# Optimization experiments

Hardware: AMD Instinct MI355X
Metric: run time of the kernel (lower is better)

## Reference

```python
import jax, jax.numpy as jnp
import numpy as np

N = 50000
E = 800000
C_IN = 256
HEADS = 4
HEAD_DIM = 32  # out_channels per head; concat=False -> final dim = HEAD_DIM


def setup_inputs() -> dict:
    key = jax.random.key(0)
    ks = jax.random.split(key, 10)
    s_in = 1.0 / np.sqrt(C_IN)
    return {
        "x": jax.random.normal(ks[0], (N, C_IN), dtype=jnp.float32),
        "edge_index": jax.random.randint(ks[1], (2, E), 0, N, dtype=jnp.int64),
        "Wq": jax.random.normal(ks[2], (C_IN, HEADS * HEAD_DIM), dtype=jnp.float32) * s_in,
        "bq": jax.random.normal(ks[3], (HEADS * HEAD_DIM,), dtype=jnp.float32) * 0.02,
        "Wk": jax.random.normal(ks[4], (C_IN, HEADS * HEAD_DIM), dtype=jnp.float32) * s_in,
        "bk": jax.random.normal(ks[5], (HEADS * HEAD_DIM,), dtype=jnp.float32) * 0.02,
        "Wv": jax.random.normal(ks[6], (C_IN, HEADS * HEAD_DIM), dtype=jnp.float32) * s_in,
        "bv": jax.random.normal(ks[7], (HEADS * HEAD_DIM,), dtype=jnp.float32) * 0.02,
        "Ws": jax.random.normal(ks[8], (C_IN, HEAD_DIM), dtype=jnp.float32) * s_in,
        "bs": jax.random.normal(ks[9], (HEAD_DIM,), dtype=jnp.float32) * 0.02,
    }


def reference(x, edge_index, Wq, bq, Wk, bk, Wv, bv, Ws, bs):
    n = x.shape[0]
    # Node-level projections, reshaped to (N, H, C)
    q = (x @ Wq + bq).reshape(n, HEADS, HEAD_DIM)
    k = (x @ Wk + bk).reshape(n, HEADS, HEAD_DIM)
    v = (x @ Wv + bv).reshape(n, HEADS, HEAD_DIM)

    src, dst = edge_index[0], edge_index[1]
    # Per-edge attention logits: (E, H)
    scale = 1.0 / jnp.sqrt(jnp.asarray(HEAD_DIM, dtype=x.dtype))
    logits = jnp.einsum("ehc,ehc->eh", q[dst], k[src]) * scale

    # Segment softmax over incoming edges of each destination node
    m = jax.ops.segment_max(logits, dst, num_segments=n)  # (N, H)
    e = jnp.exp(logits - m[dst])
    s = jax.ops.segment_sum(e, dst, num_segments=n)  # (N, H)
    alpha = e / s[dst]  # (E, H)

    # Weighted scatter-sum of values: (N, H, C)
    out = jax.ops.segment_sum(v[src] * alpha[..., None], dst, num_segments=n)
    # concat=False -> mean over heads; root skip connection
    out = out.mean(axis=1) + x @ Ws + bs  # (N, C)
    # LeakyReLU(0.1)
    return jnp.where(out > 0, out, 0.1 * out)
```

## Files before the change

### kernel.cpp

```cpp
#include <hip/hip_runtime.h>
#include <hip/hip_bf16.h>

#define NN 50000
#define EE 800000
#define CIN 256
#define HEADS 4
#define HDIM 32
#define GBM 64
#define CAP 64

typedef float f32x4 __attribute__((ext_vector_type(4)));
typedef __bf16 bf16x8 __attribute__((ext_vector_type(8)));

typedef const __attribute__((address_space(1))) unsigned int* gptr_t;
typedef __attribute__((address_space(3))) unsigned int* lptr_t;

static __device__ __forceinline__ unsigned short f2b(float f) {
    __hip_bfloat16 h = __float2bfloat16(f);
    return *(unsigned short*)&h;
}
static __device__ __forceinline__ float blo(unsigned int u) {
    union { unsigned int i; float f; } c; c.i = u << 16; return c.f;
}
static __device__ __forceinline__ float bhi(unsigned int u) {
    union { unsigned int i; float f; } c; c.i = u & 0xffff0000u; return c.f;
}

__global__ __launch_bounds__(256) void prep_w(
    const float* __restrict__ Wq, const float* __restrict__ Wk,
    const float* __restrict__ Wv, const float* __restrict__ Ws,
    unsigned short* __restrict__ WT) {
    const int t = blockIdx.x * 256 + threadIdx.x;
    if (t >= 416 * 256) return;
    const int c = t >> 8;
    const int k = t & 255;
    float w;
    if (c < 128)      w = Wq[k * 128 + c];
    else if (c < 256) w = Wk[k * 128 + (c - 128)];
    else if (c < 384) w = Wv[k * 128 + (c - 256)];
    else              w = Ws[k * 32 + (c - 384)];
    WT[t] = f2b(w);
}

__global__ __launch_bounds__(256) void mfma_gemm(
    const float* __restrict__ x, const unsigned short* __restrict__ WT,
    const float* __restrict__ bq, const float* __restrict__ bk,
    const float* __restrict__ bv, const float* __restrict__ bs,
    unsigned short* __restrict__ qb, unsigned short* __restrict__ kb,
    unsigned short* __restrict__ vb, float* __restrict__ skip) {
    __shared__ __align__(16) __hip_bfloat16 As[GBM * 256];
    __shared__ __align__(16) __hip_bfloat16 Bs[2][32 * 256];

    const int row0 = blockIdx.x * GBM;
    const int tid = threadIdx.x;
    const int wave = tid >> 6;
    const int lane = tid & 63;
    const int lr = lane & 15;
    const int lq = lane >> 4;

    #pragma unroll
    for (int i = 0; i < 8; ++i) {
        const int u = i * 256 + tid;
        const int r = u >> 5, cc = u & 31;
        int grow = row0 + r; if (grow >= NN) grow = NN - 1;
        const float4 f0 = *(const float4*)(x + (size_t)grow * CIN + cc * 8);
        const float4 f1 = *(const float4*)(x + (size_t)grow * CIN + cc * 8 + 4);
        union { unsigned short us[8]; uint4 v; } o;
        o.us[0] = f2b(f0.x); o.us[1] = f2b(f0.y); o.us[2] = f2b(f0.z); o.us[3] = f2b(f0.w);
        o.us[4] = f2b(f1.x); o.us[5] = f2b(f1.y); o.us[6] = f2b(f1.z); o.us[7] = f2b(f1.w);
        *(uint4*)(As + (r * 32 + (cc ^ (r & 7))) * 8) = o.v;
    }

    auto stageB = [&](int ct, int buf) {
        const int col0 = ct * 32;
        #pragma unroll
        for (int i = 0; i < 4; ++i) {
            const int u = i * 256 + tid;
            const int cB = u >> 5;
            const int ccs = (u & 31) ^ (cB & 7);
            __builtin_amdgcn_global_load_lds(
                (gptr_t)(const void*)(WT + (size_t)(col0 + cB) * CIN + ccs * 8),
                (lptr_t)(void*)(&Bs[buf][0] + (size_t)(i * 256 + (tid & 0xC0)) * 8),
                16, 0, 0);
        }
    };

    stageB(0, 0);
    __syncthreads();

    bf16x8 af[8];
    #pragma unroll
    for (int ks = 0; ks < 8; ++ks) {
        const int r = wave * 16 + lr;
        const int c = (ks * 4 + lq) ^ (lr & 7);
        af[ks] = *(const bf16x8*)(As + (r * 32 + c) * 8);
    }

    for (int ct = 0; ct < 13; ++ct) {
        const int cur = ct & 1;
        if (ct < 12) stageB(ct + 1, cur ^ 1);

        const int col0 = ct * 32;
        f32x4 acc[2] = {};
        #pragma unroll
        for (int ks = 0; ks < 8; ++ks) {
            const int cc = ks * 4 + lq;
            const bf16x8 b0 = *(const bf16x8*)(&Bs[cur][0] +
                (size_t)((lr * 32 + (cc ^ (lr & 7))) * 8));
            const bf16x8 b1 = *(const bf16x8*)(&Bs[cur][0] +
                (size_t)(((16 + lr) * 32 + (cc ^ (lr & 7))) * 8));
            acc[0] = __builtin_amdgcn_mfma_f32_16x16x32_bf16(af[ks], b0, acc[0], 0, 0, 0);
            acc[1] = __builtin_amdgcn_mfma_f32_16x16x32_bf16(af[ks], b1, acc[1], 0, 0, 0);
        }

        #pragma unroll
        for (int j = 0; j < 2; ++j)
            #pragma unroll
            for (int r = 0; r < 4; ++r) {
                const int grow = row0 + wave * 16 + lq * 4 + r;
                if (grow >= NN) continue;
                const int gcol = col0 + j * 16 + lr;
                const float val = acc[j][r];
                if (gcol < 128)
                    qb[(size_t)grow * 128 + gcol] = f2b(val + bq[gcol]);
                else if (gcol < 256)
                    kb[(size_t)grow * 128 + gcol - 128] = f2b(val + bk[gcol - 128]);
                else if (gcol < 384)
                    vb[(size_t)grow * 128 + gcol - 256] = f2b(val + bv[gcol - 256]);
                else
                    skip[(size_t)grow * 32 + gcol - 384] = val + bs[gcol - 384];
            }
        __syncthreads();
    }
}

__global__ __launch_bounds__(256) void fill_slots(const int* __restrict__ ei,
                                                  int* __restrict__ cnt,
                                                  unsigned short* __restrict__ slot) {
    const int t = blockIdx.x * 256 + threadIdx.x;
    if (t >= EE) return;
    const int dst = ei[EE + t];
    const int pos = atomicAdd(&cnt[dst], 1);
    if (pos < CAP) slot[(size_t)dst * CAP + pos] = (unsigned short)ei[t];
}

__global__ __launch_bounds__(256) void fused_edge(
    const unsigned short* __restrict__ qb, const unsigned short* __restrict__ kb,
    const unsigned short* __restrict__ vb, const unsigned short* __restrict__ slot,
    const int* __restrict__ cnt, const float* __restrict__ skip,
    float* __restrict__ out) {
    const int wid = blockIdx.x * 4 + (threadIdx.x >> 6);
    if (wid >= NN) return;
    const int lane = threadIdx.x & 63;
    const int sub = lane & 15;
    const int e4 = lane >> 4;

    const uint4 qu = *(const uint4*)(qb + (size_t)wid * 128 + sub * 8);
    float qf[8];
    qf[0] = blo(qu.x); qf[1] = bhi(qu.x); qf[2] = blo(qu.y); qf[3] = bhi(qu.y);
    qf[4] = blo(qu.z); qf[5] = bhi(qu.z); qf[6] = blo(qu.w); qf[7] = bhi(qu.w);

    const int deg = min(cnt[wid], CAP);
    const unsigned short* sl = slot + (size_t)wid * CAP;

    float s = 0.f;
    float acc[8] = {0.f, 0.f, 0.f, 0.f, 0.f, 0.f, 0.f, 0.f};

    for (int p0 = 0; p0 < deg; p0 += 4) {
        const int pe = p0 + e4;
        const bool valid = pe < deg;
        const int src = sl[valid ? pe : 0];
        const uint4 ku = *(const uint4*)(kb + (size_t)src * 128 + sub * 8);
        const uint4 vu = *(const uint4*)(vb + (size_t)src * 128 + sub * 8);

        float d = qf[0] * blo(ku.x) + qf[1] * bhi(ku.x)
                + qf[2] * blo(ku.y) + qf[3] * bhi(ku.y)
                + qf[4] * blo(ku.z) + qf[5] * bhi(ku.z)
                + qf[6] * blo(ku.w) + qf[7] * bhi(ku.w);
        d += __shfl_xor(d, 1);
        d += __shfl_xor(d, 2);
        const float w = valid ? __expf(d * 0.17677669529663687f) : 0.f;
        s += w;
        acc[0] += w * blo(vu.x); acc[1] += w * bhi(vu.x);
        acc[2] += w * blo(vu.y); acc[3] += w * bhi(vu.y);
        acc[4] += w * blo(vu.z); acc[5] += w * bhi(vu.z);
        acc[6] += w * blo(vu.w); acc[7] += w * bhi(vu.w);
    }

    s += __shfl_xor(s, 16); s += __shfl_xor(s, 32);
    #pragma unroll
    for (int j = 0; j < 8; ++j) {
        acc[j] += __shfl_xor(acc[j], 16);
        acc[j] += __shfl_xor(acc[j], 32);
    }
    const float inv = (s > 0.f) ? 0.25f / s : 0.f;
    #pragma unroll
    for (int j = 0; j < 8; ++j) acc[j] *= inv;
    #pragma unroll
    for (int j = 0; j < 8; ++j) {
        acc[j] += __shfl_xor(acc[j], 4);
        acc[j] += __shfl_xor(acc[j], 8);
    }

    if (lane < 4) {
        const float4 sk0 = *(const float4*)(skip + (size_t)wid * 32 + lane * 8);
        const float4 sk1 = *(const float4*)(skip + (size_t)wid * 32 + lane * 8 + 4);
        float o[8];
        o[0] = acc[0] + sk0.x; o[1] = acc[1] + sk0.y;
        o[2] = acc[2] + sk0.z; o[3] = acc[3] + sk0.w;
        o[4] = acc[4] + sk1.x; o[5] = acc[5] + sk1.y;
        o[6] = acc[6] + sk1.z; o[7] = acc[7] + sk1.w;
        #pragma unroll
        for (int j = 0; j < 8; ++j) o[j] = o[j] > 0.f ? o[j] : 0.1f * o[j];
        *(float4*)(out + (size_t)wid * 32 + lane * 8)     = make_float4(o[0], o[1], o[2], o[3]);
        *(float4*)(out + (size_t)wid * 32 + lane * 8 + 4) = make_float4(o[4], o[5], o[6], o[7]);
    }
}

extern "C" void kernel_launch(void* const* d_in, const int* in_sizes, int n_in,
                              void* d_out, int out_size, void* d_ws, size_t ws_size,
                              hipStream_t stream) {
    const float* x  = (const float*)d_in[0];
    const int*   ei = (const int*)d_in[1];
    const float* Wq = (const float*)d_in[2];
    const float* bq = (const float*)d_in[3];
    const float* Wk = (const float*)d_in[4];
    const float* bk = (const float*)d_in[5];
    const float* Wv = (const float*)d_in[6];
    const float* bv = (const float*)d_in[7];
    const float* Ws = (const float*)d_in[8];
    const float* bs = (const float*)d_in[9];
    float* out = (float*)d_out;

    char* ws = (char*)d_ws;
    size_t off = 0;
    auto alloc = [&](size_t bytes) { void* p = ws + off; off = (off + bytes + 255) & ~(size_t)255; return p; };
    unsigned short* WT   = (unsigned short*)alloc((size_t)416 * CIN * 2);
    unsigned short* qb   = (unsigned short*)alloc((size_t)NN * 128 * 2);
    unsigned short* kb   = (unsigned short*)alloc((size_t)NN * 128 * 2);
    unsigned short* vb   = (unsigned short*)alloc((size_t)NN * 128 * 2);
    float*          skip = (float*)alloc((size_t)NN * HDIM * 4);
    int*            cnt  = (int*)alloc((size_t)NN * 4);
    unsigned short* slot = (unsigned short*)alloc((size_t)NN * CAP * 2);

    hipMemsetAsync(cnt, 0, (size_t)NN * 4, stream);

    prep_w<<<(416 * 256 + 255) / 256, 256, 0, stream>>>(Wq, Wk, Wv, Ws, WT);

    fill_slots<<<(EE + 255) / 256, 256, 0, stream>>>(ei, cnt, slot);

    mfma_gemm<<<(NN + GBM - 1) / GBM, 256, 0, stream>>>(x, WT, bq, bk, bv, bs, qb, kb, vb, skip);

    fused_edge<<<(NN + 3) / 4, 256, 0, stream>>>(qb, kb, vb, slot, cnt, skip, out);
}
```

Baseline: 258.4 us.

## Stage GEMM outputs through LDS for coalesced vector stores, load A into registers

The projection GEMM now keeps all 13 column-tile accumulators in registers and writes them after the main loop, staging bf16 results (packed in pairs via lane shuffles) and fp32 skip values into a reused LDS buffer. From there each thread emits 16-byte row-contiguous stores, replacing the scattered 2-byte and 4-byte global stores that each needed bias loads and branches. The A tile is loaded straight from global into registers without an LDS round trip, and the biases are concatenated once in prep_w and cached in LDS. Holding 104 accumulator floats per thread raises register pressure, and launch_bounds(256,2) plus the 72 KB LDS footprint may limit occupancy or cause spills.

```diff
diff --git a/kernel.cpp b/kernel.cpp
--- a/kernel.cpp
+++ b/kernel.cpp
@@ -9,6 +9,10 @@
 #define GBM 64
 #define CAP 64
 
+#define OFF_C32 61440
+#define OFF_BIAS 70656
+#define LDS_BYTES 72320
+
 typedef float f32x4 __attribute__((ext_vector_type(4)));
 typedef __bf16 bf16x8 __attribute__((ext_vector_type(8)));
 
@@ -29,7 +33,9 @@
 __global__ __launch_bounds__(256) void prep_w(
     const float* __restrict__ Wq, const float* __restrict__ Wk,
     const float* __restrict__ Wv, const float* __restrict__ Ws,
-    unsigned short* __restrict__ WT) {
+    const float* __restrict__ bq, const float* __restrict__ bk,
+    const float* __restrict__ bv, const float* __restrict__ bs,
+    unsigned short* __restrict__ WT, float* __restrict__ bias_cat) {
     const int t = blockIdx.x * 256 + threadIdx.x;
     if (t >= 416 * 256) return;
     const int c = t >> 8;
@@ -40,16 +46,22 @@
     else if (c < 384) w = Wv[k * 128 + (c - 256)];
     else              w = Ws[k * 32 + (c - 384)];
     WT[t] = f2b(w);
-}
-
-__global__ __launch_bounds__(256) void mfma_gemm(
+    if (k == 0) {
+        float b;
+        if (c < 128)      b = bq[c];
+        else if (c < 256) b = bk[c - 128];
+        else if (c < 384) b = bv[c - 256];
+        else              b = bs[c - 384];
+        bias_cat[c] = b;
+    }
+}
+
+__global__ __launch_bounds__(256, 2) void mfma_gemm(
     const float* __restrict__ x, const unsigned short* __restrict__ WT,
-    const float* __restrict__ bq, const float* __restrict__ bk,
-    const float* __restrict__ bv, const float* __restrict__ bs,
+    const float* __restrict__ bias_cat,
     unsigned short* __restrict__ qb, unsigned short* __restrict__ kb,
     unsigned short* __restrict__ vb, float* __restrict__ skip) {
-    __shared__ __align__(16) __hip_bfloat16 As[GBM * 256];
-    __shared__ __align__(16) __hip_bfloat16 Bs[2][32 * 256];
+    __shared__ __align__(16) char U[LDS_BYTES];
 
     const int row0 = blockIdx.x * GBM;
     const int tid = threadIdx.x;
@@ -58,17 +70,21 @@
     const int lr = lane & 15;
     const int lq = lane >> 4;
 
-    #pragma unroll
-    for (int i = 0; i < 8; ++i) {
-        const int u = i * 256 + tid;
-        const int r = u >> 5, cc = u & 31;
-        int grow = row0 + r; if (grow >= NN) grow = NN - 1;
-        const float4 f0 = *(const float4*)(x + (size_t)grow * CIN + cc * 8);
-        const float4 f1 = *(const float4*)(x + (size_t)grow * CIN + cc * 8 + 4);
-        union { unsigned short us[8]; uint4 v; } o;
+    float* biasL = (float*)(U + OFF_BIAS);
+    for (int i = tid; i < 416; i += 256) biasL[i] = bias_cat[i];
+
+    int grow_a = row0 + wave * 16 + lr;
+    if (grow_a >= NN) grow_a = NN - 1;
+    const float* xr = x + (size_t)grow_a * CIN;
+    bf16x8 af[8];
+    #pragma unroll
+    for (int ks = 0; ks < 8; ++ks) {
+        const float4 f0 = *(const float4*)(xr + ks * 32 + lq * 8);
+        const float4 f1 = *(const float4*)(xr + ks * 32 + lq * 8 + 4);
+        union { unsigned short us[8]; bf16x8 v; } o;
         o.us[0] = f2b(f0.x); o.us[1] = f2b(f0.y); o.us[2] = f2b(f0.z); o.us[3] = f2b(f0.w);
         o.us[4] = f2b(f1.x); o.us[5] = f2b(f1.y); o.us[6] = f2b(f1.z); o.us[7] = f2b(f1.w);
-        *(uint4*)(As + (r * 32 + (cc ^ (r & 7))) * 8) = o.v;
+        af[ks] = o.v;
     }
 
     auto stageB = [&](int ct, int buf) {
@@ -80,7 +96,7 @@
             const int ccs = (u & 31) ^ (cB & 7);
             __builtin_amdgcn_global_load_lds(
                 (gptr_t)(const void*)(WT + (size_t)(col0 + cB) * CIN + ccs * 8),
-                (lptr_t)(void*)(&Bs[buf][0] + (size_t)(i * 256 + (tid & 0xC0)) * 8),
+                (lptr_t)(void*)(U + buf * 16384 + (i * 256 + (tid & 0xC0)) * 16),
                 16, 0, 0);
         }
     };
@@ -88,49 +104,72 @@
     stageB(0, 0);
     __syncthreads();
 
-    bf16x8 af[8];
-    #pragma unroll
-    for (int ks = 0; ks < 8; ++ks) {
-        const int r = wave * 16 + lr;
-        const int c = (ks * 4 + lq) ^ (lr & 7);
-        af[ks] = *(const bf16x8*)(As + (r * 32 + c) * 8);
-    }
-
+    f32x4 acc[13][2] = {};
+    #pragma unroll
     for (int ct = 0; ct < 13; ++ct) {
-        const int cur = ct & 1;
-        if (ct < 12) stageB(ct + 1, cur ^ 1);
-
-        const int col0 = ct * 32;
-        f32x4 acc[2] = {};
+        if (ct < 12) stageB(ct + 1, (ct & 1) ^ 1);
+        const unsigned short* Bc = (const unsigned short*)(U + (ct & 1) * 16384);
         #pragma unroll
         for (int ks = 0; ks < 8; ++ks) {
             const int cc = ks * 4 + lq;
-            const bf16x8 b0 = *(const bf16x8*)(&Bs[cur][0] +
-                (size_t)((lr * 32 + (cc ^ (lr & 7))) * 8));
-            const bf16x8 b1 = *(const bf16x8*)(&Bs[cur][0] +
-                (size_t)(((16 + lr) * 32 + (cc ^ (lr & 7))) * 8));
-            acc[0] = __builtin_amdgcn_mfma_f32_16x16x32_bf16(af[ks], b0, acc[0], 0, 0, 0);
-            acc[1] = __builtin_amdgcn_mfma_f32_16x16x32_bf16(af[ks], b1, acc[1], 0, 0, 0);
-        }
-
-        #pragma unroll
-        for (int j = 0; j < 2; ++j)
+            const bf16x8 b0 = *(const bf16x8*)(Bc + ((lr)      * 32 + (cc ^ (lr & 7))) * 8);
+            const bf16x8 b1 = *(const bf16x8*)(Bc + ((16 + lr) * 32 + (cc ^ (lr & 7))) * 8);
+            acc[ct][0] = __builtin_amdgcn_mfma_f32_16x16x32_bf16(af[ks], b0, acc[ct][0], 0, 0, 0);
+            acc[ct][1] = __builtin_amdgcn_mfma_f32_16x16x32_bf16(af[ks], b1, acc[ct][1], 0, 0, 0);
+        }
+        __syncthreads();
+    }
+
+    unsigned short* C16 = (unsigned short*)U;
+    float* C32 = (float*)(U + OFF_C32);
+    const int rbase = wave * 16 + lq * 4;
+    const int odd = lane & 1;
+    #pragma unroll
+    for (int ct = 0; ct < 12; ++ct) {
+        #pragma unroll
+        for (int j = 0; j < 2; ++j) {
+            const float bme = biasL[ct * 32 + j * 16 + lr];
+            unsigned int pr[4];
             #pragma unroll
             for (int r = 0; r < 4; ++r) {
-                const int grow = row0 + wave * 16 + lq * 4 + r;
-                if (grow >= NN) continue;
-                const int gcol = col0 + j * 16 + lr;
-                const float val = acc[j][r];
-                if (gcol < 128)
-                    qb[(size_t)grow * 128 + gcol] = f2b(val + bq[gcol]);
-                else if (gcol < 256)
-                    kb[(size_t)grow * 128 + gcol - 128] = f2b(val + bk[gcol - 128]);
-                else if (gcol < 384)
-                    vb[(size_t)grow * 128 + gcol - 256] = f2b(val + bv[gcol - 256]);
-                else
-                    skip[(size_t)grow * 32 + gcol - 384] = val + bs[gcol - 384];
+                const float v = acc[ct][j][r] + bme;
+                const float vn = __shfl_xor(v, 1);
+                pr[r] = odd ? ((unsigned)f2b(vn) | ((unsigned)f2b(v) << 16))
+                            : ((unsigned)f2b(v)  | ((unsigned)f2b(vn) << 16));
             }
-        __syncthreads();
+            const unsigned int w0 = odd ? pr[2] : pr[0];
+            const unsigned int w1 = odd ? pr[3] : pr[1];
+            const int colp = j * 16 + (lr & ~1);
+            const int rw = rbase + odd * 2;
+            *(unsigned int*)(C16 + ct * 2560 + (rw    ) * 40 + colp) = w0;
+            *(unsigned int*)(C16 + ct * 2560 + (rw + 1) * 40 + colp) = w1;
+        }
+    }
+    #pragma unroll
+    for (int j = 0; j < 2; ++j) {
+        const float bme = biasL[384 + j * 16 + lr];
+        #pragma unroll
+        for (int r = 0; r < 4; ++r)
+            C32[(rbase + r) * 36 + j * 16 + lr] = acc[12][j][r] + bme;
+    }
+    __syncthreads();
+
+    const int srow = tid >> 2;
+    const int schunk = tid & 3;
+    const int gr2 = row0 + srow;
+    if (gr2 < NN) {
+        #pragma unroll
+        for (int ct = 0; ct < 12; ++ct) {
+            const uint4 val = *(const uint4*)(C16 + ct * 2560 + srow * 40 + schunk * 8);
+            unsigned short* dst = (ct < 4) ? qb : (ct < 8) ? kb : vb;
+            *(uint4*)(dst + (size_t)gr2 * 128 + (ct & 3) * 32 + schunk * 8) = val;
+        }
+        #pragma unroll
+        for (int h = 0; h < 2; ++h) {
+            const int ch = schunk + h * 4;
+            const uint4 v = *(const uint4*)((const char*)C32 + srow * 144 + ch * 16);
+            *(uint4*)(skip + (size_t)gr2 * 32 + ch * 4) = v;
+        }
     }
 }
 
@@ -236,6 +275,7 @@
     size_t off = 0;
     auto alloc = [&](size_t bytes) { void* p = ws + off; off = (off + bytes + 255) & ~(size_t)255; return p; };
     unsigned short* WT   = (unsigned short*)alloc((size_t)416 * CIN * 2);
+    float*          bc   = (float*)alloc((size_t)416 * 4);
     unsigned short* qb   = (unsigned short*)alloc((size_t)NN * 128 * 2);
     unsigned short* kb   = (unsigned short*)alloc((size_t)NN * 128 * 2);
     unsigned short* vb   = (unsigned short*)alloc((size_t)NN * 128 * 2);
@@ -245,11 +285,11 @@
 
     hipMemsetAsync(cnt, 0, (size_t)NN * 4, stream);
 
-    prep_w<<<(416 * 256 + 255) / 256, 256, 0, stream>>>(Wq, Wk, Wv, Ws, WT);
+    prep_w<<<(416 * 256 + 255) / 256, 256, 0, stream>>>(Wq, Wk, Wv, Ws, bq, bk, bv, bs, WT, bc);
 
     fill_slots<<<(EE + 255) / 256, 256, 0, stream>>>(ei, cnt, slot);
 
-    mfma_gemm<<<(NN + GBM - 1) / GBM, 256, 0, stream>>>(x, WT, bq, bk, bv, bs, qb, kb, vb, skip);
+    mfma_gemm<<<(NN + GBM - 1) / GBM, 256, 0, stream>>>(x, WT, bc, qb, kb, vb, skip);
 
     fused_edge<<<(NN + 3) / 4, 256, 0, stream>>>(qb, kb, vb, slot, cnt, skip, out);
 }
```

Result: faster. 241.3 us (-6.6%).
